# Kernel optimization log

Hardware: AMD Instinct MI355X
Metric: run time of the kernel (lower is better)

## Reference

```python
import jax, jax.numpy as jnp
import numpy as np

D_MODEL = 1024
NUM_HEADS = 16
OMEGA_0 = 30.0
D_K = D_MODEL // NUM_HEADS


def _siren_uniform(key, shape, fan_in, omega_0=OMEGA_0):
    bound = np.sqrt(6.0 / fan_in) / omega_0
    return jax.random.uniform(key, shape, minval=-bound, maxval=bound, dtype=jnp.float32)


def setup_inputs() -> dict:
    key = jax.random.key(0)
    ks = jax.random.split(key, 9)
    B, S = 2, 2048
    x = jax.random.normal(ks[0], (B, S, D_MODEL), dtype=jnp.float32)
    # weights stored as (out, in) like torch nn.Linear
    Wq = _siren_uniform(ks[1], (D_MODEL, D_MODEL), D_MODEL)
    bq = _siren_uniform(ks[2], (D_MODEL,), D_MODEL)
    Wk = _siren_uniform(ks[3], (D_MODEL, D_MODEL), D_MODEL)
    bk = _siren_uniform(ks[4], (D_MODEL,), D_MODEL)
    Wv = _siren_uniform(ks[5], (D_MODEL, D_MODEL), D_MODEL)
    bv = _siren_uniform(ks[6], (D_MODEL,), D_MODEL)
    Wo = _siren_uniform(ks[7], (D_MODEL, D_MODEL), D_MODEL)
    bo = _siren_uniform(ks[8], (D_MODEL,), D_MODEL)
    return {"x": x, "Wq": Wq, "bq": bq, "Wk": Wk, "bk": bk,
            "Wv": Wv, "bv": bv, "Wo": Wo, "bo": bo}


def reference(x, Wq, bq, Wk, bk, Wv, bv, Wo, bo):
    B, S, _ = x.shape
    scale = np.sqrt(D_K).astype(np.float32)
    # project and split heads: (B, H, S, d_k)
    def proj(W, b):
        y = jnp.einsum('bsd,ed->bse', x, W) + b
        return y.reshape(B, S, NUM_HEADS, D_K).transpose(0, 2, 1, 3)
    Q = proj(Wq, bq)
    K = proj(Wk, bk)
    V = proj(Wv, bv)
    logits = jnp.einsum('bhqd,bhkd->bhqk', Q, K) / scale
    attn = jnp.sin(OMEGA_0 * logits)  # no normalization
    out = jnp.einsum('bhqk,bhkd->bhqd', attn, V)
    out = out.transpose(0, 2, 1, 3).reshape(B, S, D_MODEL)
    return jnp.einsum('bsd,ed->bse', out, Wo) + bo
```

## Files before the change

### kernel.cpp

```cpp
#include <hip/hip_runtime.h>
#include <stdint.h>

typedef __attribute__((ext_vector_type(8))) __bf16 fragAB;
typedef __attribute__((ext_vector_type(4))) float f32x4;
typedef __attribute__((ext_vector_type(16))) float f32x16;
typedef __attribute__((ext_vector_type(4))) unsigned int u32x4;

__device__ __forceinline__ unsigned short f2bf(float f) {
    union { float f; unsigned int u; } v; v.f = f;
    unsigned int u = v.u + 0x7fffu + ((v.u >> 16) & 1u);
    return (unsigned short)(u >> 16);
}

__device__ __forceinline__ f32x4 MFMA16(fragAB a, fragAB b, f32x4 c) {
    return __builtin_amdgcn_mfma_f32_16x16x32_bf16(a, b, c, 0, 0, 0);
}
__device__ __forceinline__ f32x16 MFMA32(fragAB a, fragAB b, f32x16 c) {
    return __builtin_amdgcn_mfma_f32_32x32x16_bf16(a, b, c, 0, 0, 0);
}

__device__ __forceinline__ void gl16(const void* g, void* l) {
    __builtin_amdgcn_global_load_lds((const __attribute__((address_space(1))) void*)g,
                                     (__attribute__((address_space(3))) void*)l, 16, 0, 0);
}

__device__ __forceinline__ float fsin_rev(float rev) {
    float r; asm("v_sin_f32 %0, %1" : "=v"(r) : "v"(rev)); return r;
}
__device__ __forceinline__ unsigned int cvtpk(float lo, float hi) {
    unsigned int r; asm("v_cvt_pk_bf16_f32 %0, %1, %2" : "=v"(r) : "v"(lo), "v"(hi)); return r;
}
__device__ __forceinline__ void swap32(unsigned int& a, unsigned int& b) {
    asm volatile("v_permlane32_swap_b32 %0, %1" : "+v"(a), "+v"(b));
}

#define SIN_SC 0.5968310366f

__global__ __launch_bounds__(256) void cvt_all(
    const float* __restrict__ x,  const float* __restrict__ wq, const float* __restrict__ wk,
    const float* __restrict__ wv, const float* __restrict__ wo,
    unsigned short* __restrict__ xb,  unsigned short* __restrict__ wqb, unsigned short* __restrict__ wkb,
    unsigned short* __restrict__ wvb, unsigned short* __restrict__ wob)
{
    const int bid = blockIdx.x;
    const float* s; unsigned short* d; int off;
    if (bid < 4096)      { s = x;  d = xb;  off = bid; }
    else if (bid < 5120) { s = wq; d = wqb; off = bid - 4096; }
    else if (bid < 6144) { s = wk; d = wkb; off = bid - 5120; }
    else if (bid < 7168) { s = wv; d = wvb; off = bid - 6144; }
    else                 { s = wo; d = wob; off = bid - 7168; }
    const int i = (off * 256 + threadIdx.x) * 4;
    float4 f = *(const float4*)(s + i);
    ushort4 o;
    o.x = f2bf(f.x); o.y = f2bf(f.y); o.z = f2bf(f.z); o.w = f2bf(f.w);
    *(ushort4*)(d + i) = o;
}

__global__ __launch_bounds__(256, 2)
void gemm_k(const unsigned short* __restrict__ A,
            const unsigned short* __restrict__ W0, const unsigned short* __restrict__ W1,
            const unsigned short* __restrict__ W2,
            const float* __restrict__ b0, const float* __restrict__ b1, const float* __restrict__ b2,
            void* o0, void* o1, void* o2)
{
    __shared__ unsigned short As[8192];
    __shared__ unsigned short Ws[8192];

    const int z = blockIdx.z;
    const unsigned short* W = z == 0 ? W0 : (z == 1 ? W1 : W2);
    const float* bias        = z == 0 ? b0 : (z == 1 ? b1 : b2);
    void* out                = z == 0 ? o0 : (z == 1 ? o1 : o2);

    const int t = threadIdx.x;
    const int lane = t & 63;
    const int g = lane >> 4;
    const int c = lane & 15;
    const int w = t >> 6;
    const int wm = (w >> 1) * 64;
    const int wn = (w & 1) * 64;
    const int m0 = blockIdx.y * 128;
    const int n0 = blockIdx.x * 128;

    const int srow = lane >> 3;
    const int scol = (lane & 7) * 8;

    const f32x4 zz = {0.f, 0.f, 0.f, 0.f};
    f32x4 acc[4][4];
#pragma unroll
    for (int mi = 0; mi < 4; ++mi)
#pragma unroll
        for (int ni = 0; ni < 4; ++ni) acc[mi][ni] = zz;

    for (int kt = 0; kt < 16; ++kt) {
        const int k0 = kt * 64;
#pragma unroll
        for (int r = 0; r < 4; ++r) {
            gl16(A + (size_t)(m0 + 32 * w + 8 * r + srow) * 1024 + k0 + scol,
                 (unsigned short*)As + (w * 4 + r) * 512);
            gl16(W + (size_t)(n0 + 32 * w + 8 * r + srow) * 1024 + k0 + scol,
                 (unsigned short*)Ws + (w * 4 + r) * 512);
        }
        __syncthreads();
#pragma unroll
        for (int kk = 0; kk < 2; ++kk) {
            fragAB af[4], bfr[4];
#pragma unroll
            for (int mi = 0; mi < 4; ++mi)
                af[mi] = *(const fragAB*)((char*)As + (wm + mi * 16 + c) * 128 + kk * 64 + g * 16);
#pragma unroll
            for (int ni = 0; ni < 4; ++ni)
                bfr[ni] = *(const fragAB*)((char*)Ws + (wn + ni * 16 + c) * 128 + kk * 64 + g * 16);
#pragma unroll
            for (int mi = 0; mi < 4; ++mi)
#pragma unroll
                for (int ni = 0; ni < 4; ++ni)
                    acc[mi][ni] = MFMA16(af[mi], bfr[ni], acc[mi][ni]);
        }
        __syncthreads();
    }

    float bv[4];
#pragma unroll
    for (int ni = 0; ni < 4; ++ni) bv[ni] = bias[n0 + wn + ni * 16 + c];

    if (z == 0) {
        unsigned short* C = (unsigned short*)out;
#pragma unroll
        for (int mi = 0; mi < 4; ++mi)
#pragma unroll
            for (int ni = 0; ni < 4; ++ni)
#pragma unroll
                for (int j = 0; j < 4; ++j) {
                    const int grow = m0 + wm + mi * 16 + g * 4 + j;
                    const int gcol = n0 + wn + ni * 16 + c;
                    C[(size_t)grow * 1024 + gcol] = f2bf(acc[mi][ni][j] + bv[ni]);
                }
    } else if (z == 1) {
        unsigned short* Ksh = (unsigned short*)out;
#pragma unroll
        for (int mi = 0; mi < 4; ++mi) {
            const int s0 = m0 + wm + mi * 16 + g * 4;
            const int b_ = s0 >> 11, sr = s0 & 2047;
            const int kb = sr >> 6, kbl = (sr >> 5) & 1;
            const int l31b = (mi & 1) * 16 + g * 4;
#pragma unroll
            for (int ni = 0; ni < 4; ++ni) {
                const int n = n0 + wn + ni * 16 + c;
                const int h_ = n >> 6, d = n & 63;
                const int ds = d >> 4, e = d & 7, lhalf = (d >> 3) & 1;
                const size_t base =
                    ((((size_t)(b_ * 16 + h_) * 32 + kb) * 2 + kbl) * 4 + ds) * 512
                    + lhalf * 256 + (size_t)l31b * 8 + e;
#pragma unroll
                for (int j = 0; j < 4; ++j)
                    Ksh[base + j * 8] = f2bf(acc[mi][ni][j] + bv[ni]);
            }
        }
    } else {
        unsigned short* Vsh = (unsigned short*)out;
#pragma unroll
        for (int mi = 0; mi < 4; ++mi) {
            const int s0 = m0 + wm + mi * 16 + g * 4;
            const int b_ = s0 >> 11, sr = s0 & 2047;
            const int kb = sr >> 6;
            const int kslice = mi;
            const int khalf = (g >> 1) & 1;
            const int e0 = (g & 1) * 4;
#pragma unroll
            for (int ni = 0; ni < 4; ++ni) {
                const int n = n0 + wn + ni * 16 + c;
                const int h_ = n >> 6;
                const int nei = ni >> 1;
                const int l31 = (ni & 1) * 16 + c;
                const size_t base =
                    ((((size_t)(b_ * 16 + h_) * 32 + kb) * 4 + kslice) * 2 + nei) * 512
                    + (size_t)(khalf * 32 + l31) * 8 + e0;
                ushort4 pk;
                pk.x = f2bf(acc[mi][ni][0] + bv[ni]);
                pk.y = f2bf(acc[mi][ni][1] + bv[ni]);
                pk.z = f2bf(acc[mi][ni][2] + bv[ni]);
                pk.w = f2bf(acc[mi][ni][3] + bv[ni]);
                *(ushort4*)(Vsh + base) = pk;
            }
        }
    }
}

__global__ __launch_bounds__(256, 4)
void gemm64(const unsigned short* __restrict__ A,
            const unsigned short* __restrict__ W,
            const float* __restrict__ bias, float* __restrict__ out)
{
    __shared__ unsigned short As[4096];
    __shared__ unsigned short Ws[8192];

    const int t = threadIdx.x;
    const int lane = t & 63;
    const int g = lane >> 4;
    const int c = lane & 15;
    const int w = t >> 6;
    const int wm = (w >> 1) * 32;
    const int wn = (w & 1) * 64;
    const int m0 = blockIdx.y * 64;
    const int n0 = blockIdx.x * 128;

    const int srow = lane >> 3;
    const int scol = (lane & 7) * 8;

    const f32x4 zz = {0.f, 0.f, 0.f, 0.f};
    f32x4 acc[2][4];
#pragma unroll
    for (int mi = 0; mi < 2; ++mi)
#pragma unroll
        for (int ni = 0; ni < 4; ++ni) acc[mi][ni] = zz;

    for (int kt = 0; kt < 16; ++kt) {
        const int k0 = kt * 64;
        gl16(A + (size_t)(m0 + 16 * w + srow) * 1024 + k0 + scol,
             (unsigned short*)As + (2 * w) * 512);
        gl16(A + (size_t)(m0 + 16 * w + 8 + srow) * 1024 + k0 + scol,
             (unsigned short*)As + (2 * w + 1) * 512);
#pragma unroll
        for (int r = 0; r < 4; ++r)
            gl16(W + (size_t)(n0 + 32 * w + 8 * r + srow) * 1024 + k0 + scol,
                 (unsigned short*)Ws + (w * 4 + r) * 512);
        __syncthreads();
#pragma unroll
        for (int kk = 0; kk < 2; ++kk) {
            fragAB af[2], bfr[4];
#pragma unroll
            for (int mi = 0; mi < 2; ++mi)
                af[mi] = *(const fragAB*)((char*)As + (wm + mi * 16 + c) * 128 + kk * 64 + g * 16);
#pragma unroll
            for (int ni = 0; ni < 4; ++ni)
                bfr[ni] = *(const fragAB*)((char*)Ws + (wn + ni * 16 + c) * 128 + kk * 64 + g * 16);
#pragma unroll
            for (int mi = 0; mi < 2; ++mi)
#pragma unroll
                for (int ni = 0; ni < 4; ++ni)
                    acc[mi][ni] = MFMA16(af[mi], bfr[ni], acc[mi][ni]);
        }
        __syncthreads();
    }

#pragma unroll
    for (int ni = 0; ni < 4; ++ni) {
        const float bv = bias[n0 + wn + ni * 16 + c];
#pragma unroll
        for (int mi = 0; mi < 2; ++mi)
#pragma unroll
            for (int j = 0; j < 4; ++j) {
                const int grow = m0 + wm + mi * 16 + g * 4 + j;
                const int gcol = n0 + wn + ni * 16 + c;
                out[(size_t)grow * 1024 + gcol] = acc[mi][ni][j] + bv;
            }
    }
}

__global__ __launch_bounds__(512, 2)
void attn_kernel(const unsigned short* __restrict__ Qg,
                 const unsigned short* __restrict__ Ksh,
                 const unsigned short* __restrict__ Vsh,
                 unsigned short* __restrict__ AO)
{
    __shared__ float red[16384];

    const int t = threadIdx.x;
    const int lane = t & 63;
    const int l31 = lane & 31;
    const int lh = lane >> 5;
    const int w = t >> 6;
    const int qh = w >> 1;
    const int kbl = w & 1;

    const int bid = blockIdx.x;
    const int lb = (bid & 7) * 32 + (bid >> 3);
    const int qb = lb & 7;
    const int h = (lb >> 3) & 15;
    const int b = lb >> 7;
    const int qbase = qb * 256;

    const unsigned short* Kc = Ksh + (size_t)(b * 16 + h) * 131072;
    const unsigned short* Vc = Vsh + (size_t)(b * 16 + h) * 131072;

    const unsigned short* Kw = Kc + (size_t)kbl * 2048 + lane * 8;
    const unsigned short* Vw = Vc + (size_t)kbl * 2048 + lane * 8;

    fragAB qf[2][4];
#pragma unroll
    for (int qi = 0; qi < 2; ++qi)
#pragma unroll
        for (int ds = 0; ds < 4; ++ds)
            qf[qi][ds] = *(const fragAB*)(Qg
                + (size_t)(b * 2048 + qbase + qh * 64 + qi * 32 + l31) * 1024
                + h * 64 + ds * 16 + lh * 8);

    f32x16 o[2][2];
#pragma unroll
    for (int qi = 0; qi < 2; ++qi)
#pragma unroll
        for (int ni = 0; ni < 2; ++ni)
#pragma unroll
            for (int r = 0; r < 16; ++r) o[qi][ni][r] = 0.f;

    fragAB kfA[4], vfA[4], kfB[4], vfB[4];
#pragma unroll
    for (int ds = 0; ds < 4; ++ds) kfA[ds] = *(const fragAB*)(Kw + ds * 512);
#pragma unroll
    for (int j = 0; j < 4; ++j)    vfA[j]  = *(const fragAB*)(Vw + j * 512);

    auto body = [&](int kb, fragAB (&kfc)[4], fragAB (&vfc)[4],
                            fragAB (&kfn)[4], fragAB (&vfn)[4]) {
        if (kb < 31) {
            const size_t so = (size_t)(kb + 1) * 4096;
#pragma unroll
            for (int ds = 0; ds < 4; ++ds) kfn[ds] = *(const fragAB*)(Kw + so + ds * 512);
#pragma unroll
            for (int j = 0; j < 4; ++j)    vfn[j]  = *(const fragAB*)(Vw + so + j * 512);
        }

        f32x16 st[2];
#pragma unroll
        for (int qi = 0; qi < 2; ++qi)
#pragma unroll
            for (int r = 0; r < 16; ++r) st[qi][r] = 0.f;
        __builtin_amdgcn_s_setprio(1);
#pragma unroll
        for (int qi = 0; qi < 2; ++qi)
#pragma unroll
            for (int ds = 0; ds < 4; ++ds)
                st[qi] = MFMA32(kfc[ds], qf[qi][ds], st[qi]);
        __builtin_amdgcn_s_setprio(0);

#pragma unroll
        for (int qi = 0; qi < 2; ++qi) {
            unsigned int u[8];
#pragma unroll
            for (int i = 0; i < 8; ++i)
                u[i] = cvtpk(fsin_rev(st[qi][2 * i] * SIN_SC),
                             fsin_rev(st[qi][2 * i + 1] * SIN_SC));
            swap32(u[0], u[2]); swap32(u[1], u[3]);
            swap32(u[4], u[6]); swap32(u[5], u[7]);
            union { u32x4 u; fragAB f; } pa0, pa1;
            pa0.u = (u32x4){u[0], u[1], u[2], u[3]};
            pa1.u = (u32x4){u[4], u[5], u[6], u[7]};
            __builtin_amdgcn_s_setprio(1);
#pragma unroll
            for (int ni = 0; ni < 2; ++ni) {
                o[qi][ni] = MFMA32(pa0.f, vfc[ni], o[qi][ni]);
                o[qi][ni] = MFMA32(pa1.f, vfc[2 + ni], o[qi][ni]);
            }
            __builtin_amdgcn_s_setprio(0);
        }
    };

    for (int tt = 0; tt < 16; ++tt) {
        body(2 * tt,     kfA, vfA, kfB, vfB);
        body(2 * tt + 1, kfB, vfB, kfA, vfA);
    }

    if (kbl) {
#pragma unroll
        for (int qi = 0; qi < 2; ++qi)
#pragma unroll
            for (int ni = 0; ni < 2; ++ni)
#pragma unroll
                for (int r = 0; r < 16; ++r)
                    red[(((qh * 2 + qi) * 2 + ni) * 16 + r) * 64 + lane] = o[qi][ni][r];
    }
    __syncthreads();
    if (!kbl) {
#pragma unroll
        for (int qi = 0; qi < 2; ++qi)
#pragma unroll
            for (int ni = 0; ni < 2; ++ni)
#pragma unroll
                for (int r = 0; r < 16; ++r) {
                    const float v = o[qi][ni][r]
                        + red[(((qh * 2 + qi) * 2 + ni) * 16 + r) * 64 + lane];
                    const int q = qbase + qh * 64 + qi * 32 + (r & 3) + 8 * (r >> 2) + 4 * lh;
                    AO[(size_t)(b * 2048 + q) * 1024 + h * 64 + ni * 32 + l31] = f2bf(v);
                }
    }
}

extern "C" void kernel_launch(void* const* d_in, const int* in_sizes, int n_in,
                              void* d_out, int out_size, void* d_ws, size_t ws_size,
                              hipStream_t stream) {
    (void)in_sizes; (void)n_in; (void)out_size; (void)ws_size;
    const float* x  = (const float*)d_in[0];
    const float* Wq = (const float*)d_in[1];
    const float* bq = (const float*)d_in[2];
    const float* Wk = (const float*)d_in[3];
    const float* bk = (const float*)d_in[4];
    const float* Wv = (const float*)d_in[5];
    const float* bv = (const float*)d_in[6];
    const float* Wo = (const float*)d_in[7];
    const float* bo = (const float*)d_in[8];

    char* ws = (char*)d_ws;
    unsigned short* xb    = (unsigned short*)(ws);
    unsigned short* Wqb   = (unsigned short*)(ws + (8u  << 20));
    unsigned short* Wkb   = (unsigned short*)(ws + (10u << 20));
    unsigned short* Wvb   = (unsigned short*)(ws + (12u << 20));
    unsigned short* Wob   = (unsigned short*)(ws + (14u << 20));
    unsigned short* Qb    = (unsigned short*)(ws + (16u << 20));
    unsigned short* Kshuf = (unsigned short*)(ws + (24u << 20));
    unsigned short* Vshuf = (unsigned short*)(ws + (32u << 20));
    unsigned short* AO    = (unsigned short*)(ws + (40u << 20));

    cvt_all<<<8192, 256, 0, stream>>>(x, Wq, Wk, Wv, Wo, xb, Wqb, Wkb, Wvb, Wob);

    gemm_k<<<dim3(8, 32, 3), 256, 0, stream>>>(xb, Wqb, Wkb, Wvb, bq, bk, bv,
                                               Qb, Kshuf, Vshuf);

    attn_kernel<<<256, 512, 0, stream>>>(Qb, Kshuf, Vshuf, AO);

    gemm64<<<dim3(8, 64), 256, 0, stream>>>(AO, Wob, bo, (float*)d_out);
}
```

Before: 104.1 us.

## Software-pipeline QK^T one tile ahead of sine and PV in attention

Restructures the attention inner loop so the QK^T MFMAs for the next key tile are issued before the sine evaluation and PV MFMAs of the current tile. K fragments are prefetched two tiles ahead and V one tile ahead, with score accumulators double-buffered. The aim is to overlap the VALU-heavy sine and pack work with matrix-core work and hide load latency. It also drops the s_setprio hints and raises the GEMM kernel's launch_bounds occupancy hint from 2 to 3, which adds register pressure and a risk of spills.

```diff
diff --git a/kernel.cpp b/kernel.cpp
--- a/kernel.cpp
+++ b/kernel.cpp
@@ -56,7 +56,7 @@
     *(ushort4*)(d + i) = o;
 }
 
-__global__ __launch_bounds__(256, 2)
+__global__ __launch_bounds__(256, 3)
 void gemm_k(const unsigned short* __restrict__ A,
             const unsigned short* __restrict__ W0, const unsigned short* __restrict__ W1,
             const unsigned short* __restrict__ W2,
@@ -304,59 +304,73 @@
             for (int r = 0; r < 16; ++r) o[qi][ni][r] = 0.f;
 
     fragAB kfA[4], vfA[4], kfB[4], vfB[4];
+    f32x16 stA[2], stB[2];
+
 #pragma unroll
     for (int ds = 0; ds < 4; ++ds) kfA[ds] = *(const fragAB*)(Kw + ds * 512);
 #pragma unroll
     for (int j = 0; j < 4; ++j)    vfA[j]  = *(const fragAB*)(Vw + j * 512);
-
-    auto body = [&](int kb, fragAB (&kfc)[4], fragAB (&vfc)[4],
-                            fragAB (&kfn)[4], fragAB (&vfn)[4]) {
+#pragma unroll
+    for (int qi = 0; qi < 2; ++qi)
+#pragma unroll
+        for (int r = 0; r < 16; ++r) stA[qi][r] = 0.f;
+#pragma unroll
+    for (int qi = 0; qi < 2; ++qi)
+#pragma unroll
+        for (int ds = 0; ds < 4; ++ds)
+            stA[qi] = MFMA32(kfA[ds], qf[qi][ds], stA[qi]);
+#pragma unroll
+    for (int ds = 0; ds < 4; ++ds) kfB[ds] = *(const fragAB*)(Kw + 4096 + ds * 512);
+
+    auto body = [&](int kb, fragAB (&kfn)[4], fragAB (&vfc)[4],
+                            fragAB (&kfl)[4], fragAB (&vfl)[4],
+                            f32x16 (&stc)[2], f32x16 (&stn)[2]) {
+        if (kb < 30) {
+            const size_t so = (size_t)(kb + 2) * 4096;
+#pragma unroll
+            for (int ds = 0; ds < 4; ++ds) kfl[ds] = *(const fragAB*)(Kw + so + ds * 512);
+        }
         if (kb < 31) {
             const size_t so = (size_t)(kb + 1) * 4096;
 #pragma unroll
-            for (int ds = 0; ds < 4; ++ds) kfn[ds] = *(const fragAB*)(Kw + so + ds * 512);
-#pragma unroll
-            for (int j = 0; j < 4; ++j)    vfn[j]  = *(const fragAB*)(Vw + so + j * 512);
-        }
-
-        f32x16 st[2];
-#pragma unroll
-        for (int qi = 0; qi < 2; ++qi)
-#pragma unroll
-            for (int r = 0; r < 16; ++r) st[qi][r] = 0.f;
-        __builtin_amdgcn_s_setprio(1);
-#pragma unroll
-        for (int qi = 0; qi < 2; ++qi)
-#pragma unroll
-            for (int ds = 0; ds < 4; ++ds)
-                st[qi] = MFMA32(kfc[ds], qf[qi][ds], st[qi]);
-        __builtin_amdgcn_s_setprio(0);
+            for (int j = 0; j < 4; ++j)    vfl[j]  = *(const fragAB*)(Vw + so + j * 512);
+        }
+
+        if (kb < 31) {
+#pragma unroll
+            for (int qi = 0; qi < 2; ++qi)
+#pragma unroll
+                for (int r = 0; r < 16; ++r) stn[qi][r] = 0.f;
+#pragma unroll
+            for (int qi = 0; qi < 2; ++qi)
+#pragma unroll
+                for (int ds = 0; ds < 4; ++ds)
+                    stn[qi] = MFMA32(kfn[ds], qf[qi][ds], stn[qi]);
+        }
 
 #pragma unroll
         for (int qi = 0; qi < 2; ++qi) {
             unsigned int u[8];
 #pragma unroll
             for (int i = 0; i < 8; ++i)
-                u[i] = cvtpk(fsin_rev(st[qi][2 * i] * SIN_SC),
-                             fsin_rev(st[qi][2 * i + 1] * SIN_SC));
+                u[i] = cvtpk(fsin_rev(stc[qi][2 * i] * SIN_SC),
+                             fsin_rev(stc[qi][2 * i + 1] * SIN_SC));
             swap32(u[0], u[2]); swap32(u[1], u[3]);
             swap32(u[4], u[6]); swap32(u[5], u[7]);
             union { u32x4 u; fragAB f; } pa0, pa1;
             pa0.u = (u32x4){u[0], u[1], u[2], u[3]};
             pa1.u = (u32x4){u[4], u[5], u[6], u[7]};
-            __builtin_amdgcn_s_setprio(1);
 #pragma unroll
             for (int ni = 0; ni < 2; ++ni) {
                 o[qi][ni] = MFMA32(pa0.f, vfc[ni], o[qi][ni]);
                 o[qi][ni] = MFMA32(pa1.f, vfc[2 + ni], o[qi][ni]);
             }
-            __builtin_amdgcn_s_setprio(0);
         }
     };
 
     for (int tt = 0; tt < 16; ++tt) {
-        body(2 * tt,     kfA, vfA, kfB, vfB);
-        body(2 * tt + 1, kfB, vfB, kfA, vfA);
+        body(2 * tt,     kfB, vfA, kfA, vfB, stA, stB);
+        body(2 * tt + 1, kfA, vfB, kfB, vfA, stB, stA);
     }
 
     if (kbl) {
```

Result: no change. 104.6 us (+0.5%).
